# Optimization experiments

Hardware: AMD Instinct MI355X
Metric: run time of the kernel (lower is better)

The kernel has to match this reference:

```python
import jax, jax.numpy as jnp
import numpy as np

O, T, D = 50000, 200000, 128

def setup_inputs() -> dict:
    key = jax.random.key(0)
    k1, k2, k3, k4 = jax.random.split(key, 4)
    obj_vecs = jax.random.normal(k1, (O, D), dtype=jnp.float32)
    pred_vecs = jax.random.normal(k2, (T, D), dtype=jnp.float32)
    edges = jax.random.randint(k3, (T, 2), 0, O, dtype=jnp.int64)
    W = jax.random.normal(k4, (D, D), dtype=jnp.float32) * (2.0 / D) ** 0.5
    b = jnp.zeros((D,), dtype=jnp.float32)
    return {"obj_vecs": obj_vecs, "pred_vecs": pred_vecs, "edges": edges, "W": W, "b": b}

def reference(obj_vecs, pred_vecs, edges, W, b):
    Onum, Tnum = obj_vecs.shape[0], pred_vecs.shape[0]
    N = Onum + Tnum
    # linear transform first (GCNConv: x = lin(x))
    x = jnp.concatenate([obj_vecs, pred_vecs], axis=0) @ W.T  # [N, Dout]
    k = jnp.arange(Tnum)
    # faithful to source: edges (s,k) and (k,o) -- predicate index k used directly
    loop = jnp.arange(N)
    src = jnp.concatenate([edges[:, 0], k, loop])  # [2T + N]
    dst = jnp.concatenate([k, edges[:, 1], loop])
    # symmetric GCN normalization with self-loops (weight 1)
    deg = jax.ops.segment_sum(jnp.ones(src.shape[0], x.dtype), dst, num_segments=N)
    dinv = jnp.where(deg > 0, jax.lax.rsqrt(deg), 0.0)
    norm = dinv[src] * dinv[dst]  # [E]
    msgs = x[src] * norm[:, None]  # gather + scale
    out = jax.ops.segment_sum(msgs, dst, num_segments=N) + b  # scatter-add + bias
    return out[:Onum], out[Onum:]
```

## Files before the change

kernel.cpp:

```cpp
#include <hip/hip_runtime.h>

#define O_N 50000
#define T_N 200000
#define N_N 250000
#define BCAP 32
#define OFCAP 4096

typedef __attribute__((ext_vector_type(8))) __bf16 bf16x8;
typedef __attribute__((ext_vector_type(4))) float f32x4;
typedef __attribute__((ext_vector_type(4))) unsigned short us4;

union frag_u { us4 h[2]; bf16x8 v; };

__device__ __forceinline__ unsigned short f2bf(float f) {
    union { float f; unsigned u; } v; v.f = f;
    unsigned r = v.u + 0x7FFFu + ((v.u >> 16) & 1u);
    return (unsigned short)(r >> 16);
}

__device__ __forceinline__ int swoff(int row, int k) {
    return row * 128 + ((((k >> 3) & 15) ^ (row & 7)) << 3) + (k & 7);
}

__global__ void scatter_kernel(const int* __restrict__ edges, int* __restrict__ cnt,
                               int* __restrict__ bucket, int* __restrict__ oflow_cnt,
                               int* __restrict__ oflow) {
    int t = blockIdx.x * 256 + threadIdx.x;
    if (t >= T_N) return;
    int e1 = edges[2 * t + 1];
    int pos = atomicAdd(&cnt[e1], 1);
    if (pos < BCAP) bucket[e1 * BCAP + pos] = t;
    else { int p = atomicAdd(oflow_cnt, 1); if (p < OFCAP) oflow[p] = t; }
}

__global__ void dinv_kernel(const int* __restrict__ cnt, float* __restrict__ dinv) {
    int n = blockIdx.x * 256 + threadIdx.x;
    if (n >= N_N) return;
    float deg;
    if (n < O_N)      deg = 2.0f + (float)cnt[n];
    else if (n < T_N) deg = 2.0f;
    else              deg = 1.0f;
    dinv[n] = rsqrtf(deg);
}

template<int STORE_OUT>
__launch_bounds__(256, 2)
__global__ void gemm_kernel(const float* __restrict__ src, const float* __restrict__ W,
                            const float* __restrict__ bias, float* __restrict__ dst,
                            int nodeBase, int nodeEnd, int srcNodeOff) {
    __shared__ unsigned short As[128 * 128];
    __shared__ unsigned short Ws[128 * 128];

    const int tid = threadIdx.x;
    const int tileBase = nodeBase + blockIdx.x * 128;

    for (int i = 0; i < 16; ++i) {
        int c = tid + 256 * i;
        int r = c >> 5, k4 = (c & 31) << 2;
        int gn = tileBase + r;
        float4 v = make_float4(0.f, 0.f, 0.f, 0.f);
        if (gn < nodeEnd)
            v = *(const float4*)(src + (long)(gn - srcNodeOff) * 128 + k4);
        us4 b; b.x = f2bf(v.x); b.y = f2bf(v.y); b.z = f2bf(v.z); b.w = f2bf(v.w);
        *(us4*)&As[swoff(r, k4)] = b;
    }
    for (int i = 0; i < 16; ++i) {
        int c = tid + 256 * i;
        int r = c >> 5, k4 = (c & 31) << 2;
        float4 v = *(const float4*)(W + r * 128 + k4);
        us4 b; b.x = f2bf(v.x); b.y = f2bf(v.y); b.z = f2bf(v.z); b.w = f2bf(v.w);
        *(us4*)&Ws[swoff(r, k4)] = b;
    }
    __syncthreads();

    const int w = tid >> 6, lane = tid & 63;
    const int g = lane >> 4, li = lane & 15;
    const int wr = (w >> 1) * 64, wc = (w & 1) * 64;

    const f32x4 fz = {0.f, 0.f, 0.f, 0.f};
    f32x4 acc[4][4];
    #pragma unroll
    for (int i = 0; i < 4; ++i)
        #pragma unroll
        for (int j = 0; j < 4; ++j) acc[i][j] = fz;

    #pragma unroll
    for (int kc = 0; kc < 4; ++kc) {
        const int kb = kc * 32 + g * 4;
        frag_u a[4], b[4];
        #pragma unroll
        for (int fr = 0; fr < 4; ++fr) {
            int row = wr + fr * 16 + li;
            a[fr].h[0] = *(const us4*)&As[swoff(row, kb)];
            a[fr].h[1] = *(const us4*)&As[swoff(row, kb + 16)];
        }
        #pragma unroll
        for (int fc = 0; fc < 4; ++fc) {
            int row = wc + fc * 16 + li;
            b[fc].h[0] = *(const us4*)&Ws[swoff(row, kb)];
            b[fc].h[1] = *(const us4*)&Ws[swoff(row, kb + 16)];
        }
        #pragma unroll
        for (int fr = 0; fr < 4; ++fr)
            #pragma unroll
            for (int fc = 0; fc < 4; ++fc)
                acc[fr][fc] = __builtin_amdgcn_mfma_f32_16x16x32_bf16(
                    a[fr].v, b[fc].v, acc[fr][fc], 0, 0, 0);
    }

    #pragma unroll
    for (int fr = 0; fr < 4; ++fr) {
        #pragma unroll
        for (int reg = 0; reg < 4; ++reg) {
            int row = tileBase + wr + fr * 16 + g * 4 + reg;
            if (row >= nodeEnd) continue;
            #pragma unroll
            for (int fc = 0; fc < 4; ++fc) {
                int col = wc + fc * 16 + li;
                float val = acc[fr][fc][reg];
                if (STORE_OUT) dst[(long)row * 128 + col] = val + bias[col];
                else           dst[(long)row * 128 + col] = val;
            }
        }
    }
}

__launch_bounds__(256)
__global__ void part1_kernel(const int* __restrict__ edges, const float* __restrict__ dinv,
                             const float* __restrict__ x_ws, const float* __restrict__ bias,
                             float* __restrict__ out) {
    int n = O_N + blockIdx.x * 8 + (threadIdx.x >> 5);
    if (n >= T_N) return;
    int lane = threadIdx.x & 31;
    int e0 = edges[2 * n];
    float nm = dinv[e0] * 0.70710678118654752f;
    float4 xn = ((const float4*)(x_ws + (long)n * 128))[lane];
    float4 xe = ((const float4*)(x_ws + (long)e0 * 128))[lane];
    float4 b4 = ((const float4*)bias)[lane];
    float4 o;
    o.x = b4.x + 0.5f * xn.x + nm * xe.x;
    o.y = b4.y + 0.5f * xn.y + nm * xe.y;
    o.z = b4.z + 0.5f * xn.z + nm * xe.z;
    o.w = b4.w + 0.5f * xn.w + nm * xe.w;
    ((float4*)(out + (long)n * 128))[lane] = o;
}

__launch_bounds__(256)
__global__ void gather_kernel(const int* __restrict__ edges, const int* __restrict__ cnt,
                              const int* __restrict__ bucket, const float* __restrict__ dinv,
                              const float* __restrict__ x_ws, const float* __restrict__ bias,
                              float* __restrict__ out) {
    int o = blockIdx.x * 4 + (threadIdx.x >> 6);
    if (o >= O_N) return;
    int lane = threadIdx.x & 63;
    float dio = dinv[o];

    float2 b2 = ((const float2*)bias)[lane];
    float2 xo = ((const float2*)(x_ws + (long)o * 128))[lane];
    float sn = dio * dio;
    float2 acc = make_float2(b2.x + sn * xo.x, b2.y + sn * xo.y);

    int e0 = edges[2 * o];
    float nm0 = dinv[e0] * dio;
    float2 v0 = ((const float2*)(x_ws + (long)e0 * 128))[lane];
    acc.x += v0.x * nm0; acc.y += v0.y * nm0;

    int c = cnt[o]; if (c > BCAP) c = BCAP;
    for (int i = 0; i < c; ++i) {
        int t = bucket[o * BCAP + i];
        float nm = dinv[t] * dio;
        float2 v = ((const float2*)(x_ws + (long)t * 128))[lane];
        acc.x += v.x * nm; acc.y += v.y * nm;
    }
    ((float2*)(out + (long)o * 128))[lane] = acc;
}

__launch_bounds__(256)
__global__ void oflow_kernel(const int* __restrict__ edges, const int* __restrict__ oflow_cnt,
                             const int* __restrict__ oflow, const float* __restrict__ dinv,
                             const float* __restrict__ x_ws, float* __restrict__ out) {
    int nc = *oflow_cnt; if (nc > OFCAP) nc = OFCAP;
    int gid = blockIdx.x * 8 + (threadIdx.x >> 5);
    int lane = threadIdx.x & 31;
    for (int i = gid; i < nc; i += gridDim.x * 8) {
        int t = oflow[i];
        int e1 = edges[2 * t + 1];
        float nm = dinv[t] * dinv[e1];
        float4 v = ((const float4*)(x_ws + (long)t * 128))[lane];
        float* orow = out + (long)e1 * 128 + lane * 4;
        atomicAdd(orow + 0, v.x * nm);
        atomicAdd(orow + 1, v.y * nm);
        atomicAdd(orow + 2, v.z * nm);
        atomicAdd(orow + 3, v.w * nm);
    }
}

extern "C" void kernel_launch(void* const* d_in, const int* in_sizes, int n_in,
                              void* d_out, int out_size, void* d_ws, size_t ws_size,
                              hipStream_t stream) {
    const float* obj   = (const float*)d_in[0];
    const float* pred  = (const float*)d_in[1];
    const int*   edges = (const int*)d_in[2];
    const float* W     = (const float*)d_in[3];
    const float* bias  = (const float*)d_in[4];
    float* out  = (float*)d_out;

    float* x_ws      = (float*)d_ws;
    float* dinv      = x_ws + (size_t)T_N * 128;
    int*   cnt       = (int*)(dinv + N_N);
    int*   oflow_cnt = cnt + O_N;
    int*   oflow     = oflow_cnt + 1;
    int*   bucket    = oflow + OFCAP;

    hipMemsetAsync(cnt, 0, (O_N + 1) * sizeof(int), stream);

    scatter_kernel<<<(T_N + 255) / 256, 256, 0, stream>>>(edges, cnt, bucket, oflow_cnt, oflow);
    dinv_kernel   <<<(N_N + 255) / 256, 256, 0, stream>>>(cnt, dinv);

    gemm_kernel<0><<<(O_N + 127) / 128, 256, 0, stream>>>(obj,  W, bias, x_ws, 0,    O_N, 0);
    gemm_kernel<0><<<(T_N - O_N + 127) / 128, 256, 0, stream>>>(pred, W, bias, x_ws, O_N, T_N, O_N);
    gemm_kernel<1><<<(N_N - T_N + 127) / 128, 256, 0, stream>>>(pred, W, bias, out, T_N, N_N, O_N);

    part1_kernel <<<(T_N - O_N + 7) / 8, 256, 0, stream>>>(edges, dinv, x_ws, bias, out);
    gather_kernel<<<(O_N + 3) / 4, 256, 0, stream>>>(edges, cnt, bucket, dinv, x_ws, bias, out);
    oflow_kernel <<<16, 256, 0, stream>>>(edges, oflow_cnt, oflow, dinv, x_ws, out);
}
```

Baseline: 362.6 us.

## Store transformed features in bf16, fuse predicate output into GEMM, drop LDS staging

The intermediate feature matrix x is now stored as bf16 instead of fp32, which halves the workspace writes and the gather reads in the aggregation kernels. The separate part1 kernel is folded into the predicate GEMM epilogue: each row computes its output directly from the accumulator and the gathered bf16 source row. The GEMM also loads A and W fragments straight from global memory into registers instead of staging them through swizzled LDS, and dinv is computed only for the first T nodes. The trade-off is extra rounding from bf16 storage, and fragment loads that are less coalesced and repeated per wave.

```diff
diff --git a/kernel.cpp b/kernel.cpp
--- a/kernel.cpp
+++ b/kernel.cpp
@@ -5,21 +5,23 @@
 #define N_N 250000
 #define BCAP 32
 #define OFCAP 4096
+#define INV_SQRT2 0.70710678118654752f
 
 typedef __attribute__((ext_vector_type(8))) __bf16 bf16x8;
 typedef __attribute__((ext_vector_type(4))) float f32x4;
-typedef __attribute__((ext_vector_type(4))) unsigned short us4;
-
-union frag_u { us4 h[2]; bf16x8 v; };
-
-__device__ __forceinline__ unsigned short f2bf(float f) {
-    union { float f; unsigned u; } v; v.f = f;
-    unsigned r = v.u + 0x7FFFu + ((v.u >> 16) & 1u);
-    return (unsigned short)(r >> 16);
-}
-
-__device__ __forceinline__ int swoff(int row, int k) {
-    return row * 128 + ((((k >> 3) & 15) ^ (row & 7)) << 3) + (k & 7);
+
+__device__ __forceinline__ float bf2f(unsigned short u) {
+    union { unsigned u; float f; } v; v.u = (unsigned)u << 16; return v.f;
+}
+__device__ __forceinline__ unsigned short f2bs(float f) {
+    __bf16 h = (__bf16)f;
+    union { __bf16 h; unsigned short s; } v; v.h = h; return v.s;
+}
+__device__ __forceinline__ bf16x8 mk_frag(float4 lo, float4 hi) {
+    bf16x8 r;
+    r[0] = (__bf16)lo.x; r[1] = (__bf16)lo.y; r[2] = (__bf16)lo.z; r[3] = (__bf16)lo.w;
+    r[4] = (__bf16)hi.x; r[5] = (__bf16)hi.y; r[6] = (__bf16)hi.z; r[7] = (__bf16)hi.w;
+    return r;
 }
 
 __global__ void scatter_kernel(const int* __restrict__ edges, int* __restrict__ cnt,
@@ -35,47 +37,33 @@
 
 __global__ void dinv_kernel(const int* __restrict__ cnt, float* __restrict__ dinv) {
     int n = blockIdx.x * 256 + threadIdx.x;
-    if (n >= N_N) return;
-    float deg;
-    if (n < O_N)      deg = 2.0f + (float)cnt[n];
-    else if (n < T_N) deg = 2.0f;
-    else              deg = 1.0f;
-    dinv[n] = rsqrtf(deg);
-}
-
-template<int STORE_OUT>
+    if (n >= T_N) return;
+    dinv[n] = (n < O_N) ? rsqrtf(2.0f + (float)cnt[n]) : INV_SQRT2;
+}
+
+template<int MODE>
 __launch_bounds__(256, 2)
 __global__ void gemm_kernel(const float* __restrict__ src, const float* __restrict__ W,
-                            const float* __restrict__ bias, float* __restrict__ dst,
-                            int nodeBase, int nodeEnd, int srcNodeOff) {
-    __shared__ unsigned short As[128 * 128];
-    __shared__ unsigned short Ws[128 * 128];
-
+                            const float* __restrict__ bias, const float* __restrict__ dinv,
+                            const int* __restrict__ edges,
+                            unsigned short* __restrict__ x_bf, float* __restrict__ out,
+                            int nodeBase, int nodeEnd, int srcOff) {
     const int tid = threadIdx.x;
-    const int tileBase = nodeBase + blockIdx.x * 128;
-
-    for (int i = 0; i < 16; ++i) {
-        int c = tid + 256 * i;
-        int r = c >> 5, k4 = (c & 31) << 2;
-        int gn = tileBase + r;
-        float4 v = make_float4(0.f, 0.f, 0.f, 0.f);
-        if (gn < nodeEnd)
-            v = *(const float4*)(src + (long)(gn - srcNodeOff) * 128 + k4);
-        us4 b; b.x = f2bf(v.x); b.y = f2bf(v.y); b.z = f2bf(v.z); b.w = f2bf(v.w);
-        *(us4*)&As[swoff(r, k4)] = b;
-    }
-    for (int i = 0; i < 16; ++i) {
-        int c = tid + 256 * i;
-        int r = c >> 5, k4 = (c & 31) << 2;
-        float4 v = *(const float4*)(W + r * 128 + k4);
-        us4 b; b.x = f2bf(v.x); b.y = f2bf(v.y); b.z = f2bf(v.z); b.w = f2bf(v.w);
-        *(us4*)&Ws[swoff(r, k4)] = b;
-    }
-    __syncthreads();
-
     const int w = tid >> 6, lane = tid & 63;
     const int g = lane >> 4, li = lane & 15;
     const int wr = (w >> 1) * 64, wc = (w & 1) * 64;
+    const int tileBase = nodeBase + blockIdx.x * 128;
+
+    bf16x8 bfr[4][4];
+    #pragma unroll
+    for (int fc = 0; fc < 4; ++fc) {
+        const float* wp = W + (wc + fc * 16 + li) * 128;
+        #pragma unroll
+        for (int kc = 0; kc < 4; ++kc) {
+            int kb = kc * 32 + g * 4;
+            bfr[fc][kc] = mk_frag(*(const float4*)(wp + kb), *(const float4*)(wp + kb + 16));
+        }
+    }
 
     const f32x4 fz = {0.f, 0.f, 0.f, 0.f};
     f32x4 acc[4][4];
@@ -84,28 +72,27 @@
         #pragma unroll
         for (int j = 0; j < 4; ++j) acc[i][j] = fz;
 
+    const float4 z4 = make_float4(0.f, 0.f, 0.f, 0.f);
     #pragma unroll
     for (int kc = 0; kc < 4; ++kc) {
-        const int kb = kc * 32 + g * 4;
-        frag_u a[4], b[4];
+        bf16x8 afr[4];
         #pragma unroll
         for (int fr = 0; fr < 4; ++fr) {
-            int row = wr + fr * 16 + li;
-            a[fr].h[0] = *(const us4*)&As[swoff(row, kb)];
-            a[fr].h[1] = *(const us4*)&As[swoff(row, kb + 16)];
-        }
-        #pragma unroll
-        for (int fc = 0; fc < 4; ++fc) {
-            int row = wc + fc * 16 + li;
-            b[fc].h[0] = *(const us4*)&Ws[swoff(row, kb)];
-            b[fc].h[1] = *(const us4*)&Ws[swoff(row, kb + 16)];
+            int row = tileBase + wr + fr * 16 + li;
+            float4 lo = z4, hi = z4;
+            if (row < nodeEnd) {
+                const float* ap = src + (long)(row - srcOff) * 128 + kc * 32 + g * 4;
+                lo = *(const float4*)ap;
+                hi = *(const float4*)(ap + 16);
+            }
+            afr[fr] = mk_frag(lo, hi);
         }
         #pragma unroll
         for (int fr = 0; fr < 4; ++fr)
             #pragma unroll
             for (int fc = 0; fc < 4; ++fc)
                 acc[fr][fc] = __builtin_amdgcn_mfma_f32_16x16x32_bf16(
-                    a[fr].v, b[fc].v, acc[fr][fc], 0, 0, 0);
+                    afr[fr], bfr[fc][kc], acc[fr][fc], 0, 0, 0);
     }
 
     #pragma unroll
@@ -114,63 +101,60 @@
         for (int reg = 0; reg < 4; ++reg) {
             int row = tileBase + wr + fr * 16 + g * 4 + reg;
             if (row >= nodeEnd) continue;
-            #pragma unroll
-            for (int fc = 0; fc < 4; ++fc) {
-                int col = wc + fc * 16 + li;
-                float val = acc[fr][fc][reg];
-                if (STORE_OUT) dst[(long)row * 128 + col] = val + bias[col];
-                else           dst[(long)row * 128 + col] = val;
+            if (MODE == 0) {
+                #pragma unroll
+                for (int fc = 0; fc < 4; ++fc) {
+                    int col = wc + fc * 16 + li;
+                    x_bf[(long)row * 128 + col] = f2bs(acc[fr][fc][reg]);
+                }
+            } else if (MODE == 1) {
+                int e0 = edges[2 * row];
+                float nm = dinv[e0] * INV_SQRT2;
+                const unsigned short* xe = x_bf + (long)e0 * 128;
+                #pragma unroll
+                for (int fc = 0; fc < 4; ++fc) {
+                    int col = wc + fc * 16 + li;
+                    float a = acc[fr][fc][reg];
+                    x_bf[(long)row * 128 + col] = f2bs(a);
+                    out[(long)row * 128 + col] = bias[col] + 0.5f * a + nm * bf2f(xe[col]);
+                }
+            } else {
+                #pragma unroll
+                for (int fc = 0; fc < 4; ++fc) {
+                    int col = wc + fc * 16 + li;
+                    out[(long)row * 128 + col] = acc[fr][fc][reg] + bias[col];
+                }
             }
         }
     }
-}
-
-__launch_bounds__(256)
-__global__ void part1_kernel(const int* __restrict__ edges, const float* __restrict__ dinv,
-                             const float* __restrict__ x_ws, const float* __restrict__ bias,
-                             float* __restrict__ out) {
-    int n = O_N + blockIdx.x * 8 + (threadIdx.x >> 5);
-    if (n >= T_N) return;
-    int lane = threadIdx.x & 31;
-    int e0 = edges[2 * n];
-    float nm = dinv[e0] * 0.70710678118654752f;
-    float4 xn = ((const float4*)(x_ws + (long)n * 128))[lane];
-    float4 xe = ((const float4*)(x_ws + (long)e0 * 128))[lane];
-    float4 b4 = ((const float4*)bias)[lane];
-    float4 o;
-    o.x = b4.x + 0.5f * xn.x + nm * xe.x;
-    o.y = b4.y + 0.5f * xn.y + nm * xe.y;
-    o.z = b4.z + 0.5f * xn.z + nm * xe.z;
-    o.w = b4.w + 0.5f * xn.w + nm * xe.w;
-    ((float4*)(out + (long)n * 128))[lane] = o;
 }
 
 __launch_bounds__(256)
 __global__ void gather_kernel(const int* __restrict__ edges, const int* __restrict__ cnt,
                               const int* __restrict__ bucket, const float* __restrict__ dinv,
-                              const float* __restrict__ x_ws, const float* __restrict__ bias,
-                              float* __restrict__ out) {
+                              const unsigned short* __restrict__ x_bf,
+                              const float* __restrict__ bias, float* __restrict__ out) {
     int o = blockIdx.x * 4 + (threadIdx.x >> 6);
     if (o >= O_N) return;
     int lane = threadIdx.x & 63;
     float dio = dinv[o];
 
     float2 b2 = ((const float2*)bias)[lane];
-    float2 xo = ((const float2*)(x_ws + (long)o * 128))[lane];
+    ushort2 xo = ((const ushort2*)(x_bf + (long)o * 128))[lane];
     float sn = dio * dio;
-    float2 acc = make_float2(b2.x + sn * xo.x, b2.y + sn * xo.y);
+    float2 acc = make_float2(b2.x + sn * bf2f(xo.x), b2.y + sn * bf2f(xo.y));
 
     int e0 = edges[2 * o];
     float nm0 = dinv[e0] * dio;
-    float2 v0 = ((const float2*)(x_ws + (long)e0 * 128))[lane];
-    acc.x += v0.x * nm0; acc.y += v0.y * nm0;
+    ushort2 v0 = ((const ushort2*)(x_bf + (long)e0 * 128))[lane];
+    acc.x += bf2f(v0.x) * nm0; acc.y += bf2f(v0.y) * nm0;
 
     int c = cnt[o]; if (c > BCAP) c = BCAP;
     for (int i = 0; i < c; ++i) {
         int t = bucket[o * BCAP + i];
         float nm = dinv[t] * dio;
-        float2 v = ((const float2*)(x_ws + (long)t * 128))[lane];
-        acc.x += v.x * nm; acc.y += v.y * nm;
+        ushort2 v = ((const ushort2*)(x_bf + (long)t * 128))[lane];
+        acc.x += bf2f(v.x) * nm; acc.y += bf2f(v.y) * nm;
     }
     ((float2*)(out + (long)o * 128))[lane] = acc;
 }
@@ -178,7 +162,7 @@
 __launch_bounds__(256)
 __global__ void oflow_kernel(const int* __restrict__ edges, const int* __restrict__ oflow_cnt,
                              const int* __restrict__ oflow, const float* __restrict__ dinv,
-                             const float* __restrict__ x_ws, float* __restrict__ out) {
+                             const unsigned short* __restrict__ x_bf, float* __restrict__ out) {
     int nc = *oflow_cnt; if (nc > OFCAP) nc = OFCAP;
     int gid = blockIdx.x * 8 + (threadIdx.x >> 5);
     int lane = threadIdx.x & 31;
@@ -186,12 +170,12 @@
         int t = oflow[i];
         int e1 = edges[2 * t + 1];
         float nm = dinv[t] * dinv[e1];
-        float4 v = ((const float4*)(x_ws + (long)t * 128))[lane];
+        const unsigned short* xr = x_bf + (long)t * 128 + lane * 4;
         float* orow = out + (long)e1 * 128 + lane * 4;
-        atomicAdd(orow + 0, v.x * nm);
-        atomicAdd(orow + 1, v.y * nm);
-        atomicAdd(orow + 2, v.z * nm);
-        atomicAdd(orow + 3, v.w * nm);
+        atomicAdd(orow + 0, bf2f(xr[0]) * nm);
+        atomicAdd(orow + 1, bf2f(xr[1]) * nm);
+        atomicAdd(orow + 2, bf2f(xr[2]) * nm);
+        atomicAdd(orow + 3, bf2f(xr[3]) * nm);
     }
 }
 
@@ -205,9 +189,9 @@
     const float* bias  = (const float*)d_in[4];
     float* out  = (float*)d_out;
 
-    float* x_ws      = (float*)d_ws;
-    float* dinv      = x_ws + (size_t)T_N * 128;
-    int*   cnt       = (int*)(dinv + N_N);
+    unsigned short* x_bf = (unsigned short*)d_ws;
+    float* dinv      = (float*)(x_bf + (size_t)T_N * 128);
+    int*   cnt       = (int*)(dinv + T_N);
     int*   oflow_cnt = cnt + O_N;
     int*   oflow     = oflow_cnt + 1;
     int*   bucket    = oflow + OFCAP;
@@ -215,13 +199,15 @@
     hipMemsetAsync(cnt, 0, (O_N + 1) * sizeof(int), stream);
 
     scatter_kernel<<<(T_N + 255) / 256, 256, 0, stream>>>(edges, cnt, bucket, oflow_cnt, oflow);
-    dinv_kernel   <<<(N_N + 255) / 256, 256, 0, stream>>>(cnt, dinv);
-
-    gemm_kernel<0><<<(O_N + 127) / 128, 256, 0, stream>>>(obj,  W, bias, x_ws, 0,    O_N, 0);
-    gemm_kernel<0><<<(T_N - O_N + 127) / 128, 256, 0, stream>>>(pred, W, bias, x_ws, O_N, T_N, O_N);
-    gemm_kernel<1><<<(N_N - T_N + 127) / 128, 256, 0, stream>>>(pred, W, bias, out, T_N, N_N, O_N);
-
-    part1_kernel <<<(T_N - O_N + 7) / 8, 256, 0, stream>>>(edges, dinv, x_ws, bias, out);
-    gather_kernel<<<(O_N + 3) / 4, 256, 0, stream>>>(edges, cnt, bucket, dinv, x_ws, bias, out);
-    oflow_kernel <<<16, 256, 0, stream>>>(edges, oflow_cnt, oflow, dinv, x_ws, out);
-}
+    dinv_kernel   <<<(T_N + 255) / 256, 256, 0, stream>>>(cnt, dinv);
+
+    gemm_kernel<0><<<(O_N + 127) / 128, 256, 0, stream>>>(obj, W, bias, dinv, edges,
+                                                          x_bf, out, 0, O_N, 0);
+    gemm_kernel<1><<<(T_N - O_N + 127) / 128, 256, 0, stream>>>(pred, W, bias, dinv, edges,
+                                                                x_bf, out, O_N, T_N, O_N);
+    gemm_kernel<2><<<(N_N - T_N + 127) / 128, 256, 0, stream>>>(pred, W, bias, dinv, edges,
+                                                                x_bf, out, T_N, N_N, O_N);
+
+    gather_kernel<<<(O_N + 3) / 4, 256, 0, stream>>>(edges, cnt, bucket, dinv, x_bf, bias, out);
+    oflow_kernel <<<16, 256, 0, stream>>>(edges, oflow_cnt, oflow, dinv, x_bf, out);
+}
```

Measured after the change: 370.1 us. 1.02x slower.
